# Performance work log

Measured on AMD Instinct MI355X. Metric: run time of the kernel, lower is better.

## Reference

```python
import jax, jax.numpy as jnp
import numpy as np

JITTER_EPS = 0.01  # router_jitter_noise


def sparsemixer_top2(scores, jitter_eps):
    # scores: [T, E]. Faithful port of PhiMoE sparsemixer (top_k == 2).
    E = scores.shape[-1]
    eye = jnp.arange(E)
    # ---- expert 1 ----
    max1 = jnp.max(scores, axis=-1, keepdims=True)
    ind1 = jnp.argmax(scores, axis=-1)                      # [T]
    factor1 = jnp.maximum(jnp.abs(scores), max1)            # scores.abs().clamp(min=max)
    mask1 = (max1 - scores) / factor1 > 2.0 * jitter_eps
    gates1 = jax.nn.softmax(jnp.where(mask1, -jnp.inf, scores), axis=-1)
    mult1 = jnp.take_along_axis(gates1, ind1[:, None], axis=-1)   # [T,1]
    # ---- expert 2: mask out first pick, repeat ----
    oh1 = eye[None, :] == ind1[:, None]
    masked_scores = jnp.where(oh1, -jnp.inf, scores)
    max2 = jnp.max(masked_scores, axis=-1, keepdims=True)
    ind2 = jnp.argmax(masked_scores, axis=-1)
    factor2 = jnp.maximum(jnp.abs(scores), max2)
    mask2 = (max2 - scores) / factor2 > 2.0 * jitter_eps
    gates2 = jax.nn.softmax(jnp.where(mask2, -jnp.inf, masked_scores), axis=-1)
    mult2 = jnp.take_along_axis(gates2, ind2[:, None], axis=-1)   # [T,1]
    topk_w = jnp.concatenate([mult1, mult2], axis=-1)       # [T,2]
    topk_ids = jnp.stack([ind1, ind2], axis=-1)             # [T,2]
    return topk_w, topk_ids


def setup_inputs() -> dict:
    key = jax.random.key(0)
    ks = jax.random.split(key, 5)
    B, S, D, F, E = 2, 2048, 1024, 2048, 8
    hidden_states = jax.random.normal(ks[0], (B, S, D), dtype=jnp.float32)
    gate_w = jax.random.normal(ks[1], (E, D), dtype=jnp.float32) * (D ** -0.5)
    w_gate = jax.random.normal(ks[2], (E, F, D), dtype=jnp.float32) * (D ** -0.5)
    w_up = jax.random.normal(ks[3], (E, F, D), dtype=jnp.float32) * (D ** -0.5)
    w_down = jax.random.normal(ks[4], (E, D, F), dtype=jnp.float32) * (F ** -0.5)
    return {"hidden_states": hidden_states, "gate_w": gate_w,
            "w_gate": w_gate, "w_up": w_up, "w_down": w_down}


def reference(hidden_states, gate_w, w_gate, w_up, w_down):
    B, S, D = hidden_states.shape
    E = gate_w.shape[0]
    x = hidden_states.reshape(-1, D)                         # [T,D]
    router_logits = x @ gate_w.T                             # [T,E]
    topk_w, topk_ids = sparsemixer_top2(router_logits, JITTER_EPS)
    # per-token combine weights over experts: [T,E]
    comb = jnp.sum(topk_w[:, :, None] *
                   (topk_ids[:, :, None] == jnp.arange(E)[None, None, :]).astype(topk_w.dtype),
                   axis=1)
    out = jnp.zeros_like(x)
    for e in range(E):  # small fixed expert count
        h = jax.nn.silu(x @ w_gate[e].T) * (x @ w_up[e].T)   # [T,F]
        out = out + comb[:, e:e + 1] * (h @ w_down[e].T)     # [T,D]
    return out.reshape(B, S, D), router_logits
```

## Files before the change

kernel.cpp:

```cpp
#include <hip/hip_runtime.h>
#include <stdint.h>

#define TOK    4096
#define DMODEL 1024
#define FDIM   2048
#define NEXP   8
#define MAXP   9216
#define MAXT   72
#define OUT_MAIN (TOK * DMODEL)

#define IDX_CNT 0
#define IDX_CUR 8
#define IDX_SEG 16
#define IDX_NT  24
#define IDX_TE  32
#define IDX_TR  112

#define OFF_META 0
#define OFF_TKE  1024
#define OFF_TKW  33792
#define OFF_PTOK 66560
#define OFF_PW   103424
#define OFF_XG   140288
#define OFF_H    19014656
#define OFF_WGB  56763392
#define OFF_WUB  90317824
#define OFF_WDB  123872256
#define OFF_PV   OFF_WGB
#define OFF_RPOS 157426688
#define WS_NEED  157459456

typedef __attribute__((ext_vector_type(8))) __bf16 bf16x8;
typedef __attribute__((ext_vector_type(8))) unsigned short u16x8;
typedef __attribute__((ext_vector_type(4))) unsigned short u16x4;
typedef __attribute__((ext_vector_type(4))) float f32x4;

__device__ __forceinline__ unsigned short f2bf(float f) {
  unsigned u = __builtin_bit_cast(unsigned, f);
  u += 0x7fffu + ((u >> 16) & 1u);
  return (unsigned short)(u >> 16);
}

__device__ __forceinline__ void async_load16(const void* g, void* l) {
  __builtin_amdgcn_global_load_lds(
      (__attribute__((address_space(1))) void*)g,
      (__attribute__((address_space(3))) void*)l, 16, 0, 0);
}

__device__ __forceinline__ bf16x8 ld_frag(const unsigned short* p) {
  return __builtin_bit_cast(bf16x8, *(const u16x8*)p);
}

__device__ __forceinline__ f32x4 zero4() { f32x4 z = {0.f, 0.f, 0.f, 0.f}; return z; }

__global__ void k_conv(const float* __restrict__ src, unsigned short* __restrict__ dst) {
  size_t i = ((size_t)blockIdx.x * 256 + threadIdx.x) * 8;
  float4 a = *(const float4*)(src + i);
  float4 b = *(const float4*)(src + i + 4);
  u16x8 v = {f2bf(a.x), f2bf(a.y), f2bf(a.z), f2bf(a.w),
             f2bf(b.x), f2bf(b.y), f2bf(b.z), f2bf(b.w)};
  *(u16x8*)(dst + i) = v;
}

__global__ void k_router(const float* __restrict__ x, const float* __restrict__ gw,
                         float* __restrict__ logits) {
  int lane = threadIdx.x & 63;
  int t = blockIdx.x * 4 + (threadIdx.x >> 6);
  double acc[NEXP];
#pragma unroll
  for (int e = 0; e < NEXP; ++e) acc[e] = 0.0;
  const float* xp = x + (size_t)t * DMODEL;
  for (int i = 0; i < DMODEL / 64; ++i) {
    int d = i * 64 + lane;
    float xv = xp[d];
#pragma unroll
    for (int e = 0; e < NEXP; ++e) acc[e] += (double)xv * (double)gw[e * DMODEL + d];
  }
#pragma unroll
  for (int e = 0; e < NEXP; ++e) {
    double v = acc[e];
#pragma unroll
    for (int off = 32; off > 0; off >>= 1) v += __shfl_down(v, off, 64);
    if (lane == 0) logits[t * NEXP + e] = (float)v;
  }
}

__global__ void k_routing(const float* __restrict__ logits, int* __restrict__ meta,
                          int* __restrict__ tk_e, float* __restrict__ tk_w) {
  int t = blockIdx.x * blockDim.x + threadIdx.x;
  float s[NEXP];
#pragma unroll
  for (int e = 0; e < NEXP; ++e) s[e] = logits[t * NEXP + e];
  float max1 = s[0]; int ind1 = 0;
#pragma unroll
  for (int e = 1; e < NEXP; ++e) if (s[e] > max1) { max1 = s[e]; ind1 = e; }
  float sum1 = 0.f;
#pragma unroll
  for (int e = 0; e < NEXP; ++e) {
    float f = fmaxf(fabsf(s[e]), max1);
    if (!((max1 - s[e]) / f > 0.02f)) sum1 += expf(s[e] - max1);
  }
  float w1 = 1.f / sum1;
  float max2 = -3.4e38f; int ind2 = 0;
#pragma unroll
  for (int e = 0; e < NEXP; ++e) if (e != ind1 && s[e] > max2) { max2 = s[e]; ind2 = e; }
  float sum2 = 0.f;
#pragma unroll
  for (int e = 0; e < NEXP; ++e) {
    if (e == ind1) continue;
    float f = fmaxf(fabsf(s[e]), max2);
    if (!((max2 - s[e]) / f > 0.02f)) sum2 += expf(s[e] - max2);
  }
  float w2 = 1.f / sum2;
  tk_e[2 * t] = ind1; tk_e[2 * t + 1] = ind2;
  tk_w[2 * t] = w1;   tk_w[2 * t + 1] = w2;
  atomicAdd(&meta[IDX_CNT + ind1], 1);
  atomicAdd(&meta[IDX_CNT + ind2], 1);
}

__global__ void k_scan(int* __restrict__ meta) {
  if (threadIdx.x != 0) return;
  int off = 0, nt = 0;
  for (int e = 0; e < NEXP; ++e) {
    meta[IDX_SEG + e] = off;
    int cnt = meta[IDX_CNT + e];
    int tiles = (cnt + 127) >> 7;
    for (int j = 0; j < tiles; ++j) {
      meta[IDX_TE + nt] = e;
      meta[IDX_TR + nt] = off + (j << 7);
      ++nt;
    }
    off += tiles << 7;
  }
  meta[IDX_NT] = nt;
}

__global__ void k_scatter(const int* __restrict__ tk_e, const float* __restrict__ tk_w,
                          int* __restrict__ meta, int* __restrict__ ptok,
                          float* __restrict__ pw, int* __restrict__ rpos) {
  int t = blockIdx.x * blockDim.x + threadIdx.x;
#pragma unroll
  for (int k = 0; k < 2; ++k) {
    int e = tk_e[2 * t + k];
    int p = atomicAdd(&meta[IDX_CUR + e], 1);
    int r = meta[IDX_SEG + e] + p;
    ptok[r] = t;
    pw[r] = tk_w[2 * t + k];
    rpos[2 * t + k] = r;
  }
}

__global__ void k_gather(const float* __restrict__ x, const int* __restrict__ ptok,
                         unsigned short* __restrict__ xg) {
  int r = blockIdx.x;
  int t = ptok[r];
  int c = threadIdx.x << 2;
  unsigned short o0 = 0, o1 = 0, o2 = 0, o3 = 0;
  if (t >= 0) {
    float4 v = *(const float4*)(x + ((size_t)t << 10) + c);
    o0 = f2bf(v.x); o1 = f2bf(v.y); o2 = f2bf(v.z); o3 = f2bf(v.w);
  }
  u16x4 o = {o0, o1, o2, o3};
  *(u16x4*)(xg + ((size_t)r << 10) + c) = o;
}

template <bool PRE>
__global__ __launch_bounds__(256, 3) void k_gu(
    const unsigned short* __restrict__ xg,
    const float* __restrict__ w_gate32, const float* __restrict__ w_up32,
    const unsigned short* __restrict__ w_gateb, const unsigned short* __restrict__ w_upb,
    unsigned short* __restrict__ h, const int* __restrict__ meta) {
  int nt = meta[IDX_NT];
  int rt = blockIdx.y;
  if (rt >= nt) return;
  int e = meta[IDX_TE + rt];
  int row0 = meta[IDX_TR + rt];
  int n0 = blockIdx.x * 64;

  __shared__ __align__(16) unsigned short As[8192], Bg[4096], Bu[4096];

  int tid = threadIdx.x;
  int lane = tid & 63;
  int w = tid >> 6;
  int wm = w & 1, wn = w >> 1;
  int fr = lane & 15, fq = lane >> 4;

  f32x4 accg[8], accu[8];
#pragma unroll
  for (int i = 0; i < 8; ++i) { accg[i] = zero4(); accu[i] = zero4(); }

  for (int ks = 0; ks < DMODEL / 64; ++ks) {
    int k0 = ks * 64;
    if (ks) __syncthreads();
#pragma unroll
    for (int i = 0; i < 4; ++i) {
      int c = w * 4 + i;
      int msub = c >> 1, ksub = c & 1;
      const unsigned short* gp =
          xg + (size_t)(row0 + msub * 16 + fr) * DMODEL + (k0 + ksub * 32 + fq * 8);
      async_load16(gp, &As[c * 512]);
    }
    if constexpr (PRE) {
      const unsigned short* Wg = w_gateb + (size_t)e * FDIM * DMODEL;
      const unsigned short* Wu = w_upb + (size_t)e * FDIM * DMODEL;
#pragma unroll
      for (int i = 0; i < 2; ++i) {
        int c = w * 2 + i;
        int nrow = n0 + ((c >> 1) << 4) + fr;
        int kk = k0 + ((c & 1) << 5) + (fq << 3);
        size_t off = (size_t)nrow * DMODEL + kk;
        async_load16(Wg + off, &Bg[c * 512]);
        async_load16(Wu + off, &Bu[c * 512]);
      }
    } else {
      const float* Wg = w_gate32 + (size_t)e * FDIM * DMODEL;
      const float* Wu = w_up32 + (size_t)e * FDIM * DMODEL;
#pragma unroll
      for (int i = 0; i < 2; ++i) {
        int tau = tid + 256 * i;
        int c = tau >> 6, l = tau & 63;
        int nrow = n0 + ((c >> 1) << 4) + (l & 15);
        int kk = k0 + ((c & 1) << 5) + ((l >> 4) << 3);
        const float* sg = Wg + (size_t)nrow * DMODEL + kk;
        const float* su = Wu + (size_t)nrow * DMODEL + kk;
        float4 g0 = *(const float4*)sg;
        float4 g1 = *(const float4*)(sg + 4);
        float4 u0 = *(const float4*)su;
        float4 u1 = *(const float4*)(su + 4);
        u16x8 vg = {f2bf(g0.x), f2bf(g0.y), f2bf(g0.z), f2bf(g0.w),
                    f2bf(g1.x), f2bf(g1.y), f2bf(g1.z), f2bf(g1.w)};
        u16x8 vu = {f2bf(u0.x), f2bf(u0.y), f2bf(u0.z), f2bf(u0.w),
                    f2bf(u1.x), f2bf(u1.y), f2bf(u1.z), f2bf(u1.w)};
        *(u16x8*)&Bg[c * 512 + l * 8] = vg;
        *(u16x8*)&Bu[c * 512 + l * 8] = vu;
      }
    }
    __syncthreads();
#pragma unroll
    for (int ksub = 0; ksub < 2; ++ksub) {
      bf16x8 a[4];
#pragma unroll
      for (int ms = 0; ms < 4; ++ms)
        a[ms] = ld_frag(&As[(((wm * 4 + ms) << 1) + ksub) * 512 + lane * 8]);
#pragma unroll
      for (int ns = 0; ns < 2; ++ns) {
        bf16x8 vg = ld_frag(&Bg[(((wn * 2 + ns) << 1) + ksub) * 512 + lane * 8]);
        bf16x8 vu = ld_frag(&Bu[(((wn * 2 + ns) << 1) + ksub) * 512 + lane * 8]);
#pragma unroll
        for (int ms = 0; ms < 4; ++ms) {
          accg[ms * 2 + ns] =
              __builtin_amdgcn_mfma_f32_16x16x32_bf16(a[ms], vg, accg[ms * 2 + ns], 0, 0, 0);
          accu[ms * 2 + ns] =
              __builtin_amdgcn_mfma_f32_16x16x32_bf16(a[ms], vu, accu[ms * 2 + ns], 0, 0, 0);
        }
      }
    }
  }
#pragma unroll
  for (int ms = 0; ms < 4; ++ms) {
#pragma unroll
    for (int ns = 0; ns < 2; ++ns) {
      f32x4 g4 = accg[ms * 2 + ns], u4 = accu[ms * 2 + ns];
#pragma unroll
      for (int i = 0; i < 4; ++i) {
        int lrow = wm * 64 + ms * 16 + fq * 4 + i;
        int col = n0 + wn * 32 + ns * 16 + fr;
        float gv = g4[i], uv = u4[i];
        float hv = gv * uv / (1.f + __expf(-gv));
        h[(size_t)(row0 + lrow) * FDIM + col] = f2bf(hv);
      }
    }
  }
}

template <bool PRE>
__global__ __launch_bounds__(256, 4) void k_down(
    const unsigned short* __restrict__ h, const float* __restrict__ w_down32,
    const unsigned short* __restrict__ w_downb, float* __restrict__ out,
    float* __restrict__ pv, const int* __restrict__ meta,
    const int* __restrict__ ptok, const float* __restrict__ pw) {
  int nt = meta[IDX_NT];
  int rt = blockIdx.y;
  if (rt >= nt) return;
  int e = meta[IDX_TE + rt];
  int row0 = meta[IDX_TR + rt];
  int d0 = blockIdx.x * 64;

  __shared__ __align__(16) unsigned short Ah[8192], Bd[4096];
  __shared__ int stok[128];
  __shared__ float sw[128];

  int tid = threadIdx.x;
  int lane = tid & 63;
  int w = tid >> 6;
  int wm = w & 1, wn = w >> 1;
  int fr = lane & 15, fq = lane >> 4;

  if constexpr (!PRE) {
    if (tid < 128) { stok[tid] = ptok[row0 + tid]; sw[tid] = pw[row0 + tid]; }
  }

  f32x4 acc[8];
#pragma unroll
  for (int i = 0; i < 8; ++i) acc[i] = zero4();

  for (int ks = 0; ks < FDIM / 64; ++ks) {
    int k0 = ks * 64;
    if (ks) __syncthreads();
#pragma unroll
    for (int i = 0; i < 4; ++i) {
      int c = w * 4 + i;
      int msub = c >> 1, ksub = c & 1;
      const unsigned short* gp =
          h + (size_t)(row0 + msub * 16 + fr) * FDIM + (k0 + ksub * 32 + fq * 8);
      async_load16(gp, &Ah[c * 512]);
    }
    if constexpr (PRE) {
      const unsigned short* Wd = w_downb + (size_t)e * DMODEL * FDIM;
#pragma unroll
      for (int i = 0; i < 2; ++i) {
        int c = w * 2 + i;
        int drow = d0 + ((c >> 1) << 4) + fr;
        int kk = k0 + ((c & 1) << 5) + (fq << 3);
        async_load16(Wd + (size_t)drow * FDIM + kk, &Bd[c * 512]);
      }
    } else {
      const float* Wd = w_down32 + (size_t)e * DMODEL * FDIM;
#pragma unroll
      for (int i = 0; i < 2; ++i) {
        int tau = tid + 256 * i;
        int c = tau >> 6, l = tau & 63;
        int drow = d0 + ((c >> 1) << 4) + (l & 15);
        int kk = k0 + ((c & 1) << 5) + ((l >> 4) << 3);
        const float* sd = Wd + (size_t)drow * FDIM + kk;
        float4 b0 = *(const float4*)sd;
        float4 b1 = *(const float4*)(sd + 4);
        u16x8 vb = {f2bf(b0.x), f2bf(b0.y), f2bf(b0.z), f2bf(b0.w),
                    f2bf(b1.x), f2bf(b1.y), f2bf(b1.z), f2bf(b1.w)};
        *(u16x8*)&Bd[c * 512 + l * 8] = vb;
      }
    }
    __syncthreads();
#pragma unroll
    for (int ksub = 0; ksub < 2; ++ksub) {
      bf16x8 a[4];
#pragma unroll
      for (int ms = 0; ms < 4; ++ms)
        a[ms] = ld_frag(&Ah[(((wm * 4 + ms) << 1) + ksub) * 512 + lane * 8]);
#pragma unroll
      for (int ns = 0; ns < 2; ++ns) {
        bf16x8 vb = ld_frag(&Bd[(((wn * 2 + ns) << 1) + ksub) * 512 + lane * 8]);
#pragma unroll
        for (int ms = 0; ms < 4; ++ms)
          acc[ms * 2 + ns] =
              __builtin_amdgcn_mfma_f32_16x16x32_bf16(a[ms], vb, acc[ms * 2 + ns], 0, 0, 0);
      }
    }
  }
#pragma unroll
  for (int ms = 0; ms < 4; ++ms) {
#pragma unroll
    for (int ns = 0; ns < 2; ++ns) {
      f32x4 v4 = acc[ms * 2 + ns];
#pragma unroll
      for (int i = 0; i < 4; ++i) {
        int lrow = wm * 64 + ms * 16 + fq * 4 + i;
        int col = d0 + wn * 32 + ns * 16 + fr;
        if constexpr (PRE) {
          pv[(size_t)(row0 + lrow) * DMODEL + col] = v4[i];
        } else {
          int t = stok[lrow];
          if (t >= 0) atomicAdd(&out[(size_t)t * DMODEL + col], v4[i] * sw[lrow]);
        }
      }
    }
  }
}

__global__ void k_combine(const float* __restrict__ pv, const int* __restrict__ rpos,
                          const float* __restrict__ tkw, float* __restrict__ out) {
  int t = blockIdx.x;
  int r1 = rpos[2 * t], r2 = rpos[2 * t + 1];
  float w1 = tkw[2 * t], w2 = tkw[2 * t + 1];
  int c = threadIdx.x << 2;
  float4 a = *(const float4*)(pv + (size_t)r1 * DMODEL + c);
  float4 b = *(const float4*)(pv + (size_t)r2 * DMODEL + c);
  float4 o;
  o.x = w1 * a.x + w2 * b.x;
  o.y = w1 * a.y + w2 * b.y;
  o.z = w1 * a.z + w2 * b.z;
  o.w = w1 * a.w + w2 * b.w;
  *(float4*)(out + (size_t)t * DMODEL + c) = o;
}

extern "C" void kernel_launch(void* const* d_in, const int* in_sizes, int n_in,
                              void* d_out, int out_size, void* d_ws, size_t ws_size,
                              hipStream_t stream) {
  const float* x  = (const float*)d_in[0];
  const float* gw = (const float*)d_in[1];
  const float* wg = (const float*)d_in[2];
  const float* wu = (const float*)d_in[3];
  const float* wd = (const float*)d_in[4];
  float* out = (float*)d_out;
  float* logits = out + OUT_MAIN;

  char* wsb = (char*)d_ws;
  int* meta = (int*)(wsb + OFF_META);
  int* tk_e = (int*)(wsb + OFF_TKE);
  float* tk_w = (float*)(wsb + OFF_TKW);
  int* ptok = (int*)(wsb + OFF_PTOK);
  float* pw = (float*)(wsb + OFF_PW);
  unsigned short* xg = (unsigned short*)(wsb + OFF_XG);
  unsigned short* h = (unsigned short*)(wsb + OFF_H);
  unsigned short* wgb = (unsigned short*)(wsb + OFF_WGB);
  unsigned short* wub = (unsigned short*)(wsb + OFF_WUB);
  unsigned short* wdb = (unsigned short*)(wsb + OFF_WDB);
  float* pv = (float*)(wsb + OFF_PV);
  int* rpos = (int*)(wsb + OFF_RPOS);

  bool pre = ws_size >= (size_t)WS_NEED;

  hipMemsetAsync(meta, 0, 64, stream);
  hipMemsetAsync(ptok, 0xFF, MAXP * sizeof(int), stream);
  if (!pre) {
    hipMemsetAsync(out, 0, (size_t)OUT_MAIN * sizeof(float), stream);
    hipMemsetAsync(pw, 0, MAXP * sizeof(float), stream);
  }

  if (pre) {
    k_conv<<<8192, 256, 0, stream>>>(wg, wgb);
    k_conv<<<8192, 256, 0, stream>>>(wu, wub);
    k_conv<<<8192, 256, 0, stream>>>(wd, wdb);
  }

  k_router<<<TOK / 4, 256, 0, stream>>>(x, gw, logits);
  k_routing<<<TOK / 256, 256, 0, stream>>>(logits, meta, tk_e, tk_w);
  k_scan<<<1, 64, 0, stream>>>(meta);
  k_scatter<<<TOK / 256, 256, 0, stream>>>(tk_e, tk_w, meta, ptok, pw, rpos);
  k_gather<<<MAXP, 256, 0, stream>>>(x, ptok, xg);
  if (pre) {
    k_gu<true><<<dim3(FDIM / 64, MAXT), 256, 0, stream>>>(xg, wg, wu, wgb, wub, h, meta);
    k_down<true><<<dim3(DMODEL / 64, MAXT), 256, 0, stream>>>(h, wd, wdb, out, pv, meta, ptok, pw);
    k_combine<<<TOK, 256, 0, stream>>>(pv, rpos, tk_w, out);
  } else {
    k_gu<false><<<dim3(FDIM / 64, MAXT), 256, 0, stream>>>(xg, wg, wu, wgb, wub, h, meta);
    k_down<false><<<dim3(DMODEL / 64, MAXT), 256, 0, stream>>>(h, wd, wdb, out, pv, meta, ptok, pw);
  }
}
```

Before: 590.7 us.

## Switch expert GEMMs to 32x32x16 MFMA and fuse routing/prep kernels

The gate/up and down GEMMs now use 32x32x16 bf16 MFMA with 16-wide accumulators instead of 16x16x32 tiles, with a matching LDS fragment layout and hoisted base pointers. Occupancy hints are raised. Weight conversion and the router run in one fused launch, and routing, scan and scatter are merged into a single 1024-thread block using shared-memory counters, which also removes several memsets. The aim is fewer LDS fragment loads per MFMA and less launch overhead. The cost is that routing is serialized on one block.

```diff
diff --git a/kernel.cpp b/kernel.cpp
--- a/kernel.cpp
+++ b/kernel.cpp
@@ -9,15 +9,11 @@
 #define MAXT   72
 #define OUT_MAIN (TOK * DMODEL)
 
-#define IDX_CNT 0
-#define IDX_CUR 8
-#define IDX_SEG 16
 #define IDX_NT  24
 #define IDX_TE  32
 #define IDX_TR  112
 
 #define OFF_META 0
-#define OFF_TKE  1024
 #define OFF_TKW  33792
 #define OFF_PTOK 66560
 #define OFF_PW   103424
@@ -30,10 +26,10 @@
 #define OFF_RPOS 157426688
 #define WS_NEED  157459456
 
-typedef __attribute__((ext_vector_type(8))) __bf16 bf16x8;
-typedef __attribute__((ext_vector_type(8))) unsigned short u16x8;
-typedef __attribute__((ext_vector_type(4))) unsigned short u16x4;
-typedef __attribute__((ext_vector_type(4))) float f32x4;
+typedef __attribute__((ext_vector_type(8)))  __bf16 bf16x8;
+typedef __attribute__((ext_vector_type(8)))  unsigned short u16x8;
+typedef __attribute__((ext_vector_type(4)))  unsigned short u16x4;
+typedef __attribute__((ext_vector_type(16))) float f32x16;
 
 __device__ __forceinline__ unsigned short f2bf(float f) {
   unsigned u = __builtin_bit_cast(unsigned, f);
@@ -51,21 +47,28 @@
   return __builtin_bit_cast(bf16x8, *(const u16x8*)p);
 }
 
-__device__ __forceinline__ f32x4 zero4() { f32x4 z = {0.f, 0.f, 0.f, 0.f}; return z; }
-
-__global__ void k_conv(const float* __restrict__ src, unsigned short* __restrict__ dst) {
-  size_t i = ((size_t)blockIdx.x * 256 + threadIdx.x) * 8;
-  float4 a = *(const float4*)(src + i);
-  float4 b = *(const float4*)(src + i + 4);
-  u16x8 v = {f2bf(a.x), f2bf(a.y), f2bf(a.z), f2bf(a.w),
-             f2bf(b.x), f2bf(b.y), f2bf(b.z), f2bf(b.w)};
-  *(u16x8*)(dst + i) = v;
-}
-
-__global__ void k_router(const float* __restrict__ x, const float* __restrict__ gw,
-                         float* __restrict__ logits) {
+__global__ void k_prep(const float* __restrict__ wg, const float* __restrict__ wu,
+                       const float* __restrict__ wd, unsigned short* __restrict__ wgb,
+                       unsigned short* __restrict__ wub, unsigned short* __restrict__ wdb,
+                       const float* __restrict__ x, const float* __restrict__ gw,
+                       float* __restrict__ logits, int pre) {
+  int b = blockIdx.x;
+  if (b < 24576) {
+    if (!pre) return;
+    const float* src; unsigned short* dst; int bb;
+    if (b < 8192)       { src = wg; dst = wgb; bb = b; }
+    else if (b < 16384) { src = wu; dst = wub; bb = b - 8192; }
+    else                { src = wd; dst = wdb; bb = b - 16384; }
+    size_t i = ((size_t)bb * 256 + threadIdx.x) * 8;
+    float4 a = *(const float4*)(src + i);
+    float4 c = *(const float4*)(src + i + 4);
+    u16x8 v = {f2bf(a.x), f2bf(a.y), f2bf(a.z), f2bf(a.w),
+               f2bf(c.x), f2bf(c.y), f2bf(c.z), f2bf(c.w)};
+    *(u16x8*)(dst + i) = v;
+    return;
+  }
   int lane = threadIdx.x & 63;
-  int t = blockIdx.x * 4 + (threadIdx.x >> 6);
+  int t = (b - 24576) * 4 + (threadIdx.x >> 6);
   double acc[NEXP];
 #pragma unroll
   for (int e = 0; e < NEXP; ++e) acc[e] = 0.0;
@@ -85,68 +88,72 @@
   }
 }
 
-__global__ void k_routing(const float* __restrict__ logits, int* __restrict__ meta,
-                          int* __restrict__ tk_e, float* __restrict__ tk_w) {
-  int t = blockIdx.x * blockDim.x + threadIdx.x;
-  float s[NEXP];
-#pragma unroll
-  for (int e = 0; e < NEXP; ++e) s[e] = logits[t * NEXP + e];
-  float max1 = s[0]; int ind1 = 0;
-#pragma unroll
-  for (int e = 1; e < NEXP; ++e) if (s[e] > max1) { max1 = s[e]; ind1 = e; }
-  float sum1 = 0.f;
-#pragma unroll
-  for (int e = 0; e < NEXP; ++e) {
-    float f = fmaxf(fabsf(s[e]), max1);
-    if (!((max1 - s[e]) / f > 0.02f)) sum1 += expf(s[e] - max1);
-  }
-  float w1 = 1.f / sum1;
-  float max2 = -3.4e38f; int ind2 = 0;
-#pragma unroll
-  for (int e = 0; e < NEXP; ++e) if (e != ind1 && s[e] > max2) { max2 = s[e]; ind2 = e; }
-  float sum2 = 0.f;
-#pragma unroll
-  for (int e = 0; e < NEXP; ++e) {
-    if (e == ind1) continue;
-    float f = fmaxf(fabsf(s[e]), max2);
-    if (!((max2 - s[e]) / f > 0.02f)) sum2 += expf(s[e] - max2);
-  }
-  float w2 = 1.f / sum2;
-  tk_e[2 * t] = ind1; tk_e[2 * t + 1] = ind2;
-  tk_w[2 * t] = w1;   tk_w[2 * t + 1] = w2;
-  atomicAdd(&meta[IDX_CNT + ind1], 1);
-  atomicAdd(&meta[IDX_CNT + ind2], 1);
-}
-
-__global__ void k_scan(int* __restrict__ meta) {
-  if (threadIdx.x != 0) return;
-  int off = 0, nt = 0;
-  for (int e = 0; e < NEXP; ++e) {
-    meta[IDX_SEG + e] = off;
-    int cnt = meta[IDX_CNT + e];
-    int tiles = (cnt + 127) >> 7;
-    for (int j = 0; j < tiles; ++j) {
-      meta[IDX_TE + nt] = e;
-      meta[IDX_TR + nt] = off + (j << 7);
-      ++nt;
-    }
-    off += tiles << 7;
-  }
-  meta[IDX_NT] = nt;
-}
-
-__global__ void k_scatter(const int* __restrict__ tk_e, const float* __restrict__ tk_w,
-                          int* __restrict__ meta, int* __restrict__ ptok,
-                          float* __restrict__ pw, int* __restrict__ rpos) {
-  int t = blockIdx.x * blockDim.x + threadIdx.x;
-#pragma unroll
-  for (int k = 0; k < 2; ++k) {
-    int e = tk_e[2 * t + k];
-    int p = atomicAdd(&meta[IDX_CUR + e], 1);
-    int r = meta[IDX_SEG + e] + p;
-    ptok[r] = t;
-    pw[r] = tk_w[2 * t + k];
-    rpos[2 * t + k] = r;
+__global__ __launch_bounds__(1024) void k_route2(
+    const float* __restrict__ logits, int* __restrict__ meta,
+    float* __restrict__ tk_w, int* __restrict__ ptok, float* __restrict__ pw,
+    int* __restrict__ rpos) {
+  __shared__ int cnt[NEXP], cur[NEXP], seg[NEXP];
+  int tid = threadIdx.x;
+  if (tid < NEXP) { cnt[tid] = 0; cur[tid] = 0; }
+  for (int r = tid; r < MAXP; r += 1024) ptok[r] = -1;
+  __syncthreads();
+  int i1[4], i2[4]; float w1v[4], w2v[4];
+#pragma unroll
+  for (int j = 0; j < 4; ++j) {
+    int t = tid + j * 1024;
+    float s[NEXP];
+#pragma unroll
+    for (int e = 0; e < NEXP; ++e) s[e] = logits[t * NEXP + e];
+    float max1 = s[0]; int ind1 = 0;
+#pragma unroll
+    for (int e = 1; e < NEXP; ++e) if (s[e] > max1) { max1 = s[e]; ind1 = e; }
+    float sum1 = 0.f;
+#pragma unroll
+    for (int e = 0; e < NEXP; ++e) {
+      float f = fmaxf(fabsf(s[e]), max1);
+      if (!((max1 - s[e]) / f > 0.02f)) sum1 += expf(s[e] - max1);
+    }
+    float max2 = -3.4e38f; int ind2 = 0;
+#pragma unroll
+    for (int e = 0; e < NEXP; ++e) if (e != ind1 && s[e] > max2) { max2 = s[e]; ind2 = e; }
+    float sum2 = 0.f;
+#pragma unroll
+    for (int e = 0; e < NEXP; ++e) {
+      if (e == ind1) continue;
+      float f = fmaxf(fabsf(s[e]), max2);
+      if (!((max2 - s[e]) / f > 0.02f)) sum2 += expf(s[e] - max2);
+    }
+    i1[j] = ind1; i2[j] = ind2; w1v[j] = 1.f / sum1; w2v[j] = 1.f / sum2;
+    atomicAdd(&cnt[ind1], 1);
+    atomicAdd(&cnt[ind2], 1);
+  }
+  __syncthreads();
+  if (tid == 0) {
+    int off = 0, nt2 = 0;
+    for (int e = 0; e < NEXP; ++e) {
+      seg[e] = off;
+      int tiles = (cnt[e] + 127) >> 7;
+      for (int j = 0; j < tiles; ++j) {
+        meta[IDX_TE + nt2] = e;
+        meta[IDX_TR + nt2] = off + (j << 7);
+        ++nt2;
+      }
+      off += tiles << 7;
+    }
+    meta[IDX_NT] = nt2;
+  }
+  __syncthreads();
+#pragma unroll
+  for (int j = 0; j < 4; ++j) {
+    int t = tid + j * 1024;
+    int e1 = i1[j];
+    int p1 = atomicAdd(&cur[e1], 1);
+    int r1 = seg[e1] + p1;
+    ptok[r1] = t; pw[r1] = w1v[j]; rpos[2 * t] = r1; tk_w[2 * t] = w1v[j];
+    int e2 = i2[j];
+    int p2 = atomicAdd(&cur[e2], 1);
+    int r2 = seg[e2] + p2;
+    ptok[r2] = t; pw[r2] = w2v[j]; rpos[2 * t + 1] = r2; tk_w[2 * t + 1] = w2v[j];
   }
 }
 
@@ -165,10 +172,10 @@
 }
 
 template <bool PRE>
-__global__ __launch_bounds__(256, 3) void k_gu(
+__global__ __launch_bounds__(256, 4) void k_gu(
     const unsigned short* __restrict__ xg,
-    const float* __restrict__ w_gate32, const float* __restrict__ w_up32,
-    const unsigned short* __restrict__ w_gateb, const unsigned short* __restrict__ w_upb,
+    const float* __restrict__ wg32, const float* __restrict__ wu32,
+    const unsigned short* __restrict__ wgb, const unsigned short* __restrict__ wub,
     unsigned short* __restrict__ h, const int* __restrict__ meta) {
   int nt = meta[IDX_NT];
   int rt = blockIdx.y;
@@ -179,48 +186,51 @@
 
   __shared__ __align__(16) unsigned short As[8192], Bg[4096], Bu[4096];
 
-  int tid = threadIdx.x;
-  int lane = tid & 63;
-  int w = tid >> 6;
+  int tid = threadIdx.x, lane = tid & 63, w = tid >> 6;
   int wm = w & 1, wn = w >> 1;
-  int fr = lane & 15, fq = lane >> 4;
-
-  f32x4 accg[8], accu[8];
-#pragma unroll
-  for (int i = 0; i < 8; ++i) { accg[i] = zero4(); accu[i] = zero4(); }
+  int l31 = lane & 31, lh = lane >> 5;
+
+  f32x16 accg[2], accu[2];
+#pragma unroll
+  for (int i = 0; i < 2; ++i) {
+#pragma unroll
+    for (int r = 0; r < 16; ++r) { accg[i][r] = 0.f; accu[i][r] = 0.f; }
+  }
+
+  const unsigned short* Abase =
+      xg + (size_t)(row0 + w * 32 + l31) * DMODEL + lh * 8;
+  int c0 = w * 2, c1 = c0 + 1;
+  const unsigned short* G0; const unsigned short* G1;
+  const unsigned short* U0; const unsigned short* U1;
+  if constexpr (PRE) {
+    const unsigned short* WgB = wgb + (size_t)e * FDIM * DMODEL;
+    const unsigned short* WuB = wub + (size_t)e * FDIM * DMODEL;
+    size_t o0 = (size_t)(n0 + ((c0 >> 2) << 5) + l31) * DMODEL + ((c0 & 3) << 4) + lh * 8;
+    size_t o1 = (size_t)(n0 + ((c1 >> 2) << 5) + l31) * DMODEL + ((c1 & 3) << 4) + lh * 8;
+    G0 = WgB + o0; G1 = WgB + o1; U0 = WuB + o0; U1 = WuB + o1;
+  }
 
   for (int ks = 0; ks < DMODEL / 64; ++ks) {
     int k0 = ks * 64;
     if (ks) __syncthreads();
-#pragma unroll
-    for (int i = 0; i < 4; ++i) {
-      int c = w * 4 + i;
-      int msub = c >> 1, ksub = c & 1;
-      const unsigned short* gp =
-          xg + (size_t)(row0 + msub * 16 + fr) * DMODEL + (k0 + ksub * 32 + fq * 8);
-      async_load16(gp, &As[c * 512]);
-    }
+    async_load16(Abase + k0,      &As[(w * 4 + 0) * 512]);
+    async_load16(Abase + k0 + 16, &As[(w * 4 + 1) * 512]);
+    async_load16(Abase + k0 + 32, &As[(w * 4 + 2) * 512]);
+    async_load16(Abase + k0 + 48, &As[(w * 4 + 3) * 512]);
     if constexpr (PRE) {
-      const unsigned short* Wg = w_gateb + (size_t)e * FDIM * DMODEL;
-      const unsigned short* Wu = w_upb + (size_t)e * FDIM * DMODEL;
-#pragma unroll
-      for (int i = 0; i < 2; ++i) {
-        int c = w * 2 + i;
-        int nrow = n0 + ((c >> 1) << 4) + fr;
-        int kk = k0 + ((c & 1) << 5) + (fq << 3);
-        size_t off = (size_t)nrow * DMODEL + kk;
-        async_load16(Wg + off, &Bg[c * 512]);
-        async_load16(Wu + off, &Bu[c * 512]);
-      }
+      async_load16(G0 + k0, &Bg[c0 * 512]);
+      async_load16(G1 + k0, &Bg[c1 * 512]);
+      async_load16(U0 + k0, &Bu[c0 * 512]);
+      async_load16(U1 + k0, &Bu[c1 * 512]);
     } else {
-      const float* Wg = w_gate32 + (size_t)e * FDIM * DMODEL;
-      const float* Wu = w_up32 + (size_t)e * FDIM * DMODEL;
-#pragma unroll
-      for (int i = 0; i < 2; ++i) {
-        int tau = tid + 256 * i;
+      const float* Wg = wg32 + (size_t)e * FDIM * DMODEL;
+      const float* Wu = wu32 + (size_t)e * FDIM * DMODEL;
+#pragma unroll
+      for (int i2 = 0; i2 < 2; ++i2) {
+        int tau = tid + 256 * i2;
         int c = tau >> 6, l = tau & 63;
-        int nrow = n0 + ((c >> 1) << 4) + (l & 15);
-        int kk = k0 + ((c & 1) << 5) + ((l >> 4) << 3);
+        int nrow = n0 + ((c >> 2) << 5) + (l & 31);
+        int kk = k0 + ((c & 3) << 4) + ((l >> 5) << 3);
         const float* sg = Wg + (size_t)nrow * DMODEL + kk;
         const float* su = Wu + (size_t)nrow * DMODEL + kk;
         float4 g0 = *(const float4*)sg;
@@ -237,46 +247,34 @@
     }
     __syncthreads();
 #pragma unroll
-    for (int ksub = 0; ksub < 2; ++ksub) {
-      bf16x8 a[4];
-#pragma unroll
-      for (int ms = 0; ms < 4; ++ms)
-        a[ms] = ld_frag(&As[(((wm * 4 + ms) << 1) + ksub) * 512 + lane * 8]);
-#pragma unroll
-      for (int ns = 0; ns < 2; ++ns) {
-        bf16x8 vg = ld_frag(&Bg[(((wn * 2 + ns) << 1) + ksub) * 512 + lane * 8]);
-        bf16x8 vu = ld_frag(&Bu[(((wn * 2 + ns) << 1) + ksub) * 512 + lane * 8]);
-#pragma unroll
-        for (int ms = 0; ms < 4; ++ms) {
-          accg[ms * 2 + ns] =
-              __builtin_amdgcn_mfma_f32_16x16x32_bf16(a[ms], vg, accg[ms * 2 + ns], 0, 0, 0);
-          accu[ms * 2 + ns] =
-              __builtin_amdgcn_mfma_f32_16x16x32_bf16(a[ms], vu, accu[ms * 2 + ns], 0, 0, 0);
-        }
-      }
-    }
-  }
-#pragma unroll
-  for (int ms = 0; ms < 4; ++ms) {
-#pragma unroll
-    for (int ns = 0; ns < 2; ++ns) {
-      f32x4 g4 = accg[ms * 2 + ns], u4 = accu[ms * 2 + ns];
-#pragma unroll
-      for (int i = 0; i < 4; ++i) {
-        int lrow = wm * 64 + ms * 16 + fq * 4 + i;
-        int col = n0 + wn * 32 + ns * 16 + fr;
-        float gv = g4[i], uv = u4[i];
-        float hv = gv * uv / (1.f + __expf(-gv));
-        h[(size_t)(row0 + lrow) * FDIM + col] = f2bf(hv);
-      }
+    for (int kq = 0; kq < 4; ++kq) {
+      bf16x8 a0 = ld_frag(&As[((wm * 2 + 0) * 4 + kq) * 512 + lane * 8]);
+      bf16x8 a1 = ld_frag(&As[((wm * 2 + 1) * 4 + kq) * 512 + lane * 8]);
+      bf16x8 vg = ld_frag(&Bg[(wn * 4 + kq) * 512 + lane * 8]);
+      bf16x8 vu = ld_frag(&Bu[(wn * 4 + kq) * 512 + lane * 8]);
+      accg[0] = __builtin_amdgcn_mfma_f32_32x32x16_bf16(a0, vg, accg[0], 0, 0, 0);
+      accg[1] = __builtin_amdgcn_mfma_f32_32x32x16_bf16(a1, vg, accg[1], 0, 0, 0);
+      accu[0] = __builtin_amdgcn_mfma_f32_32x32x16_bf16(a0, vu, accu[0], 0, 0, 0);
+      accu[1] = __builtin_amdgcn_mfma_f32_32x32x16_bf16(a1, vu, accu[1], 0, 0, 0);
+    }
+  }
+  int col = n0 + wn * 32 + l31;
+#pragma unroll
+  for (int mt = 0; mt < 2; ++mt) {
+#pragma unroll
+    for (int r = 0; r < 16; ++r) {
+      int lrow = wm * 64 + mt * 32 + (r & 3) + ((r >> 2) << 3) + lh * 4;
+      float gv = accg[mt][r], uv = accu[mt][r];
+      float hv = gv * uv / (1.f + __expf(-gv));
+      h[(size_t)(row0 + lrow) * FDIM + col] = f2bf(hv);
     }
   }
 }
 
 template <bool PRE>
-__global__ __launch_bounds__(256, 4) void k_down(
-    const unsigned short* __restrict__ h, const float* __restrict__ w_down32,
-    const unsigned short* __restrict__ w_downb, float* __restrict__ out,
+__global__ __launch_bounds__(256, 5) void k_down(
+    const unsigned short* __restrict__ h, const float* __restrict__ wd32,
+    const unsigned short* __restrict__ wdb, float* __restrict__ out,
     float* __restrict__ pv, const int* __restrict__ meta,
     const int* __restrict__ ptok, const float* __restrict__ pw) {
   int nt = meta[IDX_NT];
@@ -290,48 +288,49 @@
   __shared__ int stok[128];
   __shared__ float sw[128];
 
-  int tid = threadIdx.x;
-  int lane = tid & 63;
-  int w = tid >> 6;
+  int tid = threadIdx.x, lane = tid & 63, w = tid >> 6;
   int wm = w & 1, wn = w >> 1;
-  int fr = lane & 15, fq = lane >> 4;
+  int l31 = lane & 31, lh = lane >> 5;
 
   if constexpr (!PRE) {
     if (tid < 128) { stok[tid] = ptok[row0 + tid]; sw[tid] = pw[row0 + tid]; }
   }
 
-  f32x4 acc[8];
-#pragma unroll
-  for (int i = 0; i < 8; ++i) acc[i] = zero4();
+  f32x16 acc[2];
+#pragma unroll
+  for (int i = 0; i < 2; ++i) {
+#pragma unroll
+    for (int r = 0; r < 16; ++r) acc[i][r] = 0.f;
+  }
+
+  const unsigned short* Abase =
+      h + (size_t)(row0 + w * 32 + l31) * FDIM + lh * 8;
+  int c0 = w * 2, c1 = c0 + 1;
+  const unsigned short* D0; const unsigned short* D1;
+  if constexpr (PRE) {
+    const unsigned short* WdB = wdb + (size_t)e * DMODEL * FDIM;
+    D0 = WdB + (size_t)(d0 + ((c0 >> 2) << 5) + l31) * FDIM + ((c0 & 3) << 4) + lh * 8;
+    D1 = WdB + (size_t)(d0 + ((c1 >> 2) << 5) + l31) * FDIM + ((c1 & 3) << 4) + lh * 8;
+  }
 
   for (int ks = 0; ks < FDIM / 64; ++ks) {
     int k0 = ks * 64;
     if (ks) __syncthreads();
-#pragma unroll
-    for (int i = 0; i < 4; ++i) {
-      int c = w * 4 + i;
-      int msub = c >> 1, ksub = c & 1;
-      const unsigned short* gp =
-          h + (size_t)(row0 + msub * 16 + fr) * FDIM + (k0 + ksub * 32 + fq * 8);
-      async_load16(gp, &Ah[c * 512]);
-    }
+    async_load16(Abase + k0,      &Ah[(w * 4 + 0) * 512]);
+    async_load16(Abase + k0 + 16, &Ah[(w * 4 + 1) * 512]);
+    async_load16(Abase + k0 + 32, &Ah[(w * 4 + 2) * 512]);
+    async_load16(Abase + k0 + 48, &Ah[(w * 4 + 3) * 512]);
     if constexpr (PRE) {
-      const unsigned short* Wd = w_downb + (size_t)e * DMODEL * FDIM;
-#pragma unroll
-      for (int i = 0; i < 2; ++i) {
-        int c = w * 2 + i;
-        int drow = d0 + ((c >> 1) << 4) + fr;
-        int kk = k0 + ((c & 1) << 5) + (fq << 3);
-        async_load16(Wd + (size_t)drow * FDIM + kk, &Bd[c * 512]);
-      }
+      async_load16(D0 + k0, &Bd[c0 * 512]);
+      async_load16(D1 + k0, &Bd[c1 * 512]);
     } else {
-      const float* Wd = w_down32 + (size_t)e * DMODEL * FDIM;
-#pragma unroll
-      for (int i = 0; i < 2; ++i) {
-        int tau = tid + 256 * i;
+      const float* Wd = wd32 + (size_t)e * DMODEL * FDIM;
+#pragma unroll
+      for (int i2 = 0; i2 < 2; ++i2) {
+        int tau = tid + 256 * i2;
         int c = tau >> 6, l = tau & 63;
-        int drow = d0 + ((c >> 1) << 4) + (l & 15);
-        int kk = k0 + ((c & 1) << 5) + ((l >> 4) << 3);
+        int drow = d0 + ((c >> 2) << 5) + (l & 31);
+        int kk = k0 + ((c & 3) << 4) + ((l >> 5) << 3);
         const float* sd = Wd + (size_t)drow * FDIM + kk;
         float4 b0 = *(const float4*)sd;
         float4 b1 = *(const float4*)(sd + 4);
@@ -342,36 +341,25 @@
     }
     __syncthreads();
 #pragma unroll
-    for (int ksub = 0; ksub < 2; ++ksub) {
-      bf16x8 a[4];
-#pragma unroll
-      for (int ms = 0; ms < 4; ++ms)
-        a[ms] = ld_frag(&Ah[(((wm * 4 + ms) << 1) + ksub) * 512 + lane * 8]);
-#pragma unroll
-      for (int ns = 0; ns < 2; ++ns) {
-        bf16x8 vb = ld_frag(&Bd[(((wn * 2 + ns) << 1) + ksub) * 512 + lane * 8]);
-#pragma unroll
-        for (int ms = 0; ms < 4; ++ms)
-          acc[ms * 2 + ns] =
-              __builtin_amdgcn_mfma_f32_16x16x32_bf16(a[ms], vb, acc[ms * 2 + ns], 0, 0, 0);
-      }
-    }
-  }
-#pragma unroll
-  for (int ms = 0; ms < 4; ++ms) {
-#pragma unroll
-    for (int ns = 0; ns < 2; ++ns) {
-      f32x4 v4 = acc[ms * 2 + ns];
-#pragma unroll
-      for (int i = 0; i < 4; ++i) {
-        int lrow = wm * 64 + ms * 16 + fq * 4 + i;
-        int col = d0 + wn * 32 + ns * 16 + fr;
-        if constexpr (PRE) {
-          pv[(size_t)(row0 + lrow) * DMODEL + col] = v4[i];
-        } else {
-          int t = stok[lrow];
-          if (t >= 0) atomicAdd(&out[(size_t)t * DMODEL + col], v4[i] * sw[lrow]);
-        }
+    for (int kq = 0; kq < 4; ++kq) {
+      bf16x8 a0 = ld_frag(&Ah[((wm * 2 + 0) * 4 + kq) * 512 + lane * 8]);
+      bf16x8 a1 = ld_frag(&Ah[((wm * 2 + 1) * 4 + kq) * 512 + lane * 8]);
+      bf16x8 vb = ld_frag(&Bd[(wn * 4 + kq) * 512 + lane * 8]);
+      acc[0] = __builtin_amdgcn_mfma_f32_32x32x16_bf16(a0, vb, acc[0], 0, 0, 0);
+      acc[1] = __builtin_amdgcn_mfma_f32_32x32x16_bf16(a1, vb, acc[1], 0, 0, 0);
+    }
+  }
+  int col = d0 + wn * 32 + l31;
+#pragma unroll
+  for (int mt = 0; mt < 2; ++mt) {
+#pragma unroll
+    for (int r = 0; r < 16; ++r) {
+      int lrow = wm * 64 + mt * 32 + (r & 3) + ((r >> 2) << 3) + lh * 4;
+      if constexpr (PRE) {
+        pv[(size_t)(row0 + lrow) * DMODEL + col] = acc[mt][r];
+      } else {
+        int t = stok[lrow];
+        if (t >= 0) atomicAdd(&out[(size_t)t * DMODEL + col], acc[mt][r] * sw[lrow]);
       }
     }
   }
@@ -406,7 +394,6 @@
 
   char* wsb = (char*)d_ws;
   int* meta = (int*)(wsb + OFF_META);
-  int* tk_e = (int*)(wsb + OFF_TKE);
   float* tk_w = (float*)(wsb + OFF_TKW);
   int* ptok = (int*)(wsb + OFF_PTOK);
   float* pw = (float*)(wsb + OFF_PW);
@@ -419,24 +406,10 @@
   int* rpos = (int*)(wsb + OFF_RPOS);
 
   bool pre = ws_size >= (size_t)WS_NEED;
-
-  hipMemsetAsync(meta, 0, 64, stream);
-  hipMemsetAsync(ptok, 0xFF, MAXP * sizeof(int), stream);
-  if (!pre) {
-    hipMemsetAsync(out, 0, (size_t)OUT_MAIN * sizeof(float), stream);
-    hipMemsetAsync(pw, 0, MAXP * sizeof(float), stream);
-  }
-
-  if (pre) {
-    k_conv<<<8192, 256, 0, stream>>>(wg, wgb);
-    k_conv<<<8192, 256, 0, stream>>>(wu, wub);
-    k_conv<<<8192, 256, 0, stream>>>(wd, wdb);
-  }
-
-  k_router<<<TOK / 4, 256, 0, stream>>>(x, gw, logits);
-  k_routing<<<TOK / 256, 256, 0, stream>>>(logits, meta, tk_e, tk_w);
-  k_scan<<<1, 64, 0, stream>>>(meta);
-  k_scatter<<<TOK / 256, 256, 0, stream>>>(tk_e, tk_w, meta, ptok, pw, rpos);
+  if (!pre) hipMemsetAsync(out, 0, (size_t)OUT_MAIN * sizeof(float), stream);
+
+  k_prep<<<25600, 256, 0, stream>>>(wg, wu, wd, wgb, wub, wdb, x, gw, logits, (int)pre);
+  k_route2<<<1, 1024, 0, stream>>>(logits, meta, tk_w, ptok, pw, rpos);
   k_gather<<<MAXP, 256, 0, stream>>>(x, ptok, xg);
   if (pre) {
     k_gu<true><<<dim3(FDIM / 64, MAXT), 256, 0, stream>>>(xg, wg, wu, wgb, wub, h, meta);
```

After: 520.1 us. 1.14x faster.
